# Optimization experiments

Measured on AMD Instinct MI355X. Metric: run time of the kernel, lower is better.

## Reference

```python
import jax, jax.numpy as jnp
import numpy as np

ED = 1024   # encoder_dim
GH = 1024   # gnn_hidden
NL = 3      # gnn_layers
NH = 8      # gnn_heads
HD = GH // NH
N = 2048    # graph nodes
B = 1024    # query/doc batch
TEMP = 0.05
LAPW = 0.1

def _layernorm(x, g, b):
    mu = jnp.mean(x, axis=-1, keepdims=True)
    var = jnp.mean((x - mu) ** 2, axis=-1, keepdims=True)
    return (x - mu) * jax.lax.rsqrt(var + 1e-5) * g + b

def _mlp_proj(x, W1, b1, g, beta, W2, b2):
    h = _layernorm(x @ W1 + b1, g, beta)
    h = jax.nn.gelu(h, approximate=False)
    return h @ W2 + b2

def _l2norm(x):
    n = jnp.linalg.norm(x, axis=-1, keepdims=True)
    return x / jnp.maximum(n, 1e-12)

def _gnn(x, adj, gatW, a1, a2, ln_g, ln_b, poW, pob):
    mask = adj > 0
    for l in range(NL):
        Wh = jnp.einsum('nf,hfo->hno', x, gatW[l])            # [H,N,HD]
        # a([Wh_i, Wh_j]) == Wh_i@a1 + Wh_j@a2 (linear, no bias): avoids NxNx2F concat
        s1 = jnp.einsum('hno,ho->hn', Wh, a1[l])
        s2 = jnp.einsum('hno,ho->hn', Wh, a2[l])
        e = jax.nn.leaky_relu(s1[:, :, None] + s2[:, None, :], 0.2)  # [H,N,N]
        att = jax.nn.softmax(jnp.where(mask[None], e, -9e15), axis=-1)
        h = jnp.einsum('hnm,hmo->hno', att, Wh)               # [H,N,HD]
        h = jnp.transpose(h, (1, 0, 2)).reshape(x.shape[0], GH)  # concat heads
        h = jax.nn.elu(_layernorm(h, ln_g[l], ln_b[l]))
        x = x + h  # in_features == hidden so residual applies every layer
    return x @ poW + pob

def _forward(query_embeds, pos_doc_embeds, node_embeds, adj, laplacian, params):
    (qW1, qb1, qg, qbt, qW2, qb2,
     dW1, db1, dg, dbt, dW2, db2,
     gatW, a1, a2, ln_g, ln_b, poW, pob) = params
    graph_embeds = _gnn(node_embeds, adj, gatW, a1, a2, ln_g, ln_b, poW, pob)
    q = _l2norm(_mlp_proj(query_embeds, qW1, qb1, qg, qbt, qW2, qb2))
    p = _l2norm(_mlp_proj(pos_doc_embeds, dW1, db1, dg, dbt, dW2, db2))
    pos_sim = jnp.sum(q * p, axis=-1) / TEMP                  # [B]
    neg_sim = (q @ p.T) / TEMP                                # [B,B]
    logits = jnp.concatenate([pos_sim[:, None], neg_sim], axis=1)
    info_nce = jnp.mean(jax.nn.logsumexp(logits, axis=-1) - logits[:, 0])
    lap = jnp.sum(graph_embeds * (laplacian @ graph_embeds)) / graph_embeds.shape[0]
    return info_nce + LAPW * lap, info_nce, lap

def setup_inputs() -> dict:
    key = jax.random.key(0)
    ks = jax.random.split(key, 24)
    r = lambda k, s: jax.random.normal(k, s, jnp.float32) * 0.02
    adj = (jax.random.uniform(ks[3], (N, N)) < 0.02).astype(jnp.float32)
    adj = jnp.maximum(adj, jnp.eye(N, dtype=jnp.float32))
    return {
        'query_embeds': jax.random.normal(ks[0], (B, ED), jnp.float32),
        'pos_doc_embeds': jax.random.normal(ks[1], (B, ED), jnp.float32),
        'node_embeds': jax.random.normal(ks[2], (N, ED), jnp.float32),
        'adj': adj,
        'laplacian': r(ks[4], (N, N)),
        'qW1': r(ks[5], (ED, ED)), 'qb1': jnp.zeros((ED,), jnp.float32),
        'qg': jnp.ones((ED,), jnp.float32), 'qbt': jnp.zeros((ED,), jnp.float32),
        'qW2': r(ks[6], (ED, ED)), 'qb2': jnp.zeros((ED,), jnp.float32),
        'dW1': r(ks[7], (ED, ED)), 'db1': jnp.zeros((ED,), jnp.float32),
        'dg': jnp.ones((ED,), jnp.float32), 'dbt': jnp.zeros((ED,), jnp.float32),
        'dW2': r(ks[8], (ED, ED)), 'db2': jnp.zeros((ED,), jnp.float32),
        'gatW': r(ks[9], (NL, NH, ED, HD)),
        'a1': r(ks[10], (NL, NH, HD)),
        'a2': r(ks[11], (NL, NH, HD)),
        'ln_g': jnp.ones((NL, GH), jnp.float32),
        'ln_b': jnp.zeros((NL, GH), jnp.float32),
        'poW': r(ks[12], (GH, ED)),
        'pob': jnp.zeros((ED,), jnp.float32),
    }

def reference(query_embeds, pos_doc_embeds, node_embeds, adj, laplacian,
              qW1, qb1, qg, qbt, qW2, qb2,
              dW1, db1, dg, dbt, dW2, db2,
              gatW, a1, a2, ln_g, ln_b, poW, pob):
    params = (qW1, qb1, qg, qbt, qW2, qb2,
              dW1, db1, dg, dbt, dW2, db2,
              gatW, a1, a2, ln_g, ln_b, poW, pob)
    return _forward(query_embeds, pos_doc_embeds, node_embeds, adj, laplacian, params)
```

## Files before the change

kernel.cpp:

```cpp
#include <hip/hip_runtime.h>
#include <math.h>

#define ED    1024
#define GH    1024
#define NLAY  3
#define NHEAD 8
#define HD    128
#define NNODE 2048
#define BQ    1024
#define CAP   192

typedef unsigned short u16;
typedef __attribute__((ext_vector_type(8))) short short8;
typedef __attribute__((ext_vector_type(4))) float f32x4;

static const size_t OFF_X    = 0;
static const size_t OFF_XB   = 2097152;
static const size_t OFF_WHB  = 3145728;
static const size_t OFF_WTG  = 4194304;
static const size_t OFF_WTPO = 5767168;
static const size_t OFF_WTQ1 = 6291456;
static const size_t OFF_WTD1 = 6815744;
static const size_t OFF_WTQ2 = 7340032;
static const size_t OFF_WTD2 = 7864320;
static const size_t OFF_G    = 8388608;
static const size_t OFF_GT   = 10485760;
static const size_t OFF_QPB  = 11534336;
static const size_t OFF_HF   = 12582912;
static const size_t OFF_HB   = 14680064;
static const size_t OFF_FF   = 15728640;
static const size_t OFF_FB   = 17825792;
static const size_t OFF_NEG  = 18874368;
static const size_t OFF_ACC  = 19922944;
static const size_t OFF_NCNT = 19922952;
static const size_t OFF_NBR  = 19925000;

__device__ __forceinline__ u16 f2bf(float f) {
  unsigned int u = __float_as_uint(f);
  return (u16)((u + 0x7fffu + ((u >> 16) & 1u)) >> 16);
}
__device__ __forceinline__ float bf2f(u16 u) {
  return __uint_as_float(((unsigned int)u) << 16);
}

__device__ __forceinline__ float waveSum(float v) {
#pragma unroll
  for (int off = 32; off; off >>= 1) v += __shfl_xor(v, off, 64);
  return v;
}
__device__ __forceinline__ float waveMax(float v) {
#pragma unroll
  for (int off = 32; off; off >>= 1) v = fmaxf(v, __shfl_xor(v, off, 64));
  return v;
}
__device__ __forceinline__ float blockSum(float v) {
  __shared__ float buf[4];
  int lane = threadIdx.x & 63, wid = threadIdx.x >> 6, nw = (blockDim.x + 63) >> 6;
  v = waveSum(v);
  __syncthreads();
  if (lane == 0) buf[wid] = v;
  __syncthreads();
  float r = buf[0];
  for (int i = 1; i < nw; ++i) r += buf[i];
  return r;
}
__device__ __forceinline__ float blockMax(float v) {
  __shared__ float buf[4];
  int lane = threadIdx.x & 63, wid = threadIdx.x >> 6, nw = (blockDim.x + 63) >> 6;
  v = waveMax(v);
  __syncthreads();
  if (lane == 0) buf[wid] = v;
  __syncthreads();
  float r = buf[0];
  for (int i = 1; i < nw; ++i) r = fmaxf(r, buf[i]);
  return r;
}

__global__ __launch_bounds__(256) void gemm128(
    const u16* __restrict__ A, const u16* __restrict__ B0,
    const u16* __restrict__ B1, float* __restrict__ C, u16* __restrict__ Cb,
    const float* __restrict__ bias0, const float* __restrict__ bias1,
    int M, int N, int K, int split, float scale) {
  __shared__ u16 As[2][128][32];
  __shared__ u16 Bs[2][128][32];
  const int tid = threadIdx.x, wave = tid >> 6, lane = tid & 63;
  const int bm = blockIdx.y * 128, bn = blockIdx.x * 128;
  const u16* Bt = (bm < split) ? B0 : B1;
  const float* bias = (bm < split) ? bias0 : bias1;

  const int sr = tid >> 2, ss = tid & 3;
  const u16* ga0 = A  + (size_t)(bm + sr) * K + ss * 8;
  const u16* ga1 = A  + (size_t)(bm + sr + 64) * K + ss * 8;
  const u16* gb0 = Bt + (size_t)(bn + sr) * K + ss * 8;
  const u16* gb1 = Bt + (size_t)(bn + sr + 64) * K + ss * 8;

  const int r16 = lane & 15, kg = lane >> 4;
  const int wm = (wave >> 1) * 64, wn = (wave & 1) * 64;

  f32x4 acc[4][4] = {};
  const int nk = K >> 5;

  float4 pa0 = *(const float4*)ga0;
  float4 pa1 = *(const float4*)ga1;
  float4 pb0 = *(const float4*)gb0;
  float4 pb1 = *(const float4*)gb1;

  for (int kt = 0; kt < nk; ++kt) {
    const int p = kt & 1;
    *(float4*)&As[p][sr][ss * 8]      = pa0;
    *(float4*)&As[p][sr + 64][ss * 8] = pa1;
    *(float4*)&Bs[p][sr][ss * 8]      = pb0;
    *(float4*)&Bs[p][sr + 64][ss * 8] = pb1;
    __syncthreads();
    if (kt + 1 < nk) {
      ga0 += 32; ga1 += 32; gb0 += 32; gb1 += 32;
      pa0 = *(const float4*)ga0;
      pa1 = *(const float4*)ga1;
      pb0 = *(const float4*)gb0;
      pb1 = *(const float4*)gb1;
    }
    short8 av[4], bv[4];
#pragma unroll
    for (int i = 0; i < 4; ++i)
      av[i] = *(const short8*)&As[p][wm + i * 16 + r16][kg * 8];
#pragma unroll
    for (int j = 0; j < 4; ++j)
      bv[j] = *(const short8*)&Bs[p][wn + j * 16 + r16][kg * 8];
#pragma unroll
    for (int i = 0; i < 4; ++i)
#pragma unroll
      for (int j = 0; j < 4; ++j)
        acc[i][j] = __builtin_amdgcn_mfma_f32_16x16x32_bf16(av[i], bv[j], acc[i][j], 0, 0, 0);
  }

  if (C) {
#pragma unroll
    for (int j = 0; j < 4; ++j) {
      int col = bn + wn + j * 16 + r16;
      float bvv = bias ? bias[col] : 0.f;
#pragma unroll
      for (int i = 0; i < 4; ++i) {
        int row0 = bm + wm + i * 16 + kg * 4;
        float* cp = C + (size_t)row0 * N + col;
#pragma unroll
        for (int r = 0; r < 4; ++r)
          cp[(size_t)r * N] = acc[i][j][r] * scale + bvv;
      }
    }
  }
  if (Cb) {
#pragma unroll
    for (int j = 0; j < 4; ++j) {
      int col = bn + wn + j * 16 + r16;
      float bvv = bias ? bias[col] : 0.f;
#pragma unroll
      for (int i = 0; i < 4; ++i) {
        int row0 = bm + wm + i * 16 + kg * 4;
        u16* cp = Cb + (size_t)row0 * N + col;
#pragma unroll
        for (int r = 0; r < 4; ++r)
          cp[(size_t)r * N] = f2bf(acc[i][j][r] * scale + bvv);
      }
    }
  }
}

__global__ __launch_bounds__(256) void gemm_dual(
    const u16* __restrict__ A0, const u16* __restrict__ B00,
    const u16* __restrict__ B01, float* __restrict__ C0, u16* __restrict__ D0,
    const float* __restrict__ e0, const float* __restrict__ f0, int M0, int sp0, float sc0,
    const u16* __restrict__ A1, const u16* __restrict__ B10,
    const u16* __restrict__ B11, float* __restrict__ C1, u16* __restrict__ D1,
    const float* __restrict__ e1, const float* __restrict__ f1, int M1, int sp1, float sc1) {
  const int z = blockIdx.z;
  const u16* A   = z ? A1 : A0;
  const u16* Bt0 = z ? B10 : B00;
  const u16* Bt1 = z ? B11 : B01;
  float* C = z ? C1 : C0;
  u16*   D = z ? D1 : D0;
  const float* bias0 = z ? e1 : e0;
  const float* bias1 = z ? f1 : f0;
  const int M = z ? M1 : M0, split = z ? sp1 : sp0;
  const float scale = z ? sc1 : sc0;
  const int bm = blockIdx.y * 128, bn = blockIdx.x * 128;
  if (bm >= M) return;
  const int N = 1024, K = 1024;
  const u16* Bt = (bm < split) ? Bt0 : Bt1;
  const float* bias = (bm < split) ? bias0 : bias1;

  __shared__ u16 As[2][128][32];
  __shared__ u16 Bs[2][128][32];
  const int tid = threadIdx.x, wave = tid >> 6, lane = tid & 63;
  const int sr = tid >> 2, ss = tid & 3;
  const u16* ga0 = A  + (size_t)(bm + sr) * K + ss * 8;
  const u16* ga1 = A  + (size_t)(bm + sr + 64) * K + ss * 8;
  const u16* gb0 = Bt + (size_t)(bn + sr) * K + ss * 8;
  const u16* gb1 = Bt + (size_t)(bn + sr + 64) * K + ss * 8;
  const int r16 = lane & 15, kg = lane >> 4;
  const int wm = (wave >> 1) * 64, wn = (wave & 1) * 64;

  f32x4 acc[4][4] = {};
  const int nk = 32;

  float4 pa0 = *(const float4*)ga0;
  float4 pa1 = *(const float4*)ga1;
  float4 pb0 = *(const float4*)gb0;
  float4 pb1 = *(const float4*)gb1;

  for (int kt = 0; kt < nk; ++kt) {
    const int p = kt & 1;
    *(float4*)&As[p][sr][ss * 8]      = pa0;
    *(float4*)&As[p][sr + 64][ss * 8] = pa1;
    *(float4*)&Bs[p][sr][ss * 8]      = pb0;
    *(float4*)&Bs[p][sr + 64][ss * 8] = pb1;
    __syncthreads();
    if (kt + 1 < nk) {
      ga0 += 32; ga1 += 32; gb0 += 32; gb1 += 32;
      pa0 = *(const float4*)ga0;
      pa1 = *(const float4*)ga1;
      pb0 = *(const float4*)gb0;
      pb1 = *(const float4*)gb1;
    }
    short8 av[4], bv[4];
#pragma unroll
    for (int i = 0; i < 4; ++i)
      av[i] = *(const short8*)&As[p][wm + i * 16 + r16][kg * 8];
#pragma unroll
    for (int j = 0; j < 4; ++j)
      bv[j] = *(const short8*)&Bs[p][wn + j * 16 + r16][kg * 8];
#pragma unroll
    for (int i = 0; i < 4; ++i)
#pragma unroll
      for (int j = 0; j < 4; ++j)
        acc[i][j] = __builtin_amdgcn_mfma_f32_16x16x32_bf16(av[i], bv[j], acc[i][j], 0, 0, 0);
  }

  if (C) {
#pragma unroll
    for (int j = 0; j < 4; ++j) {
      int col = bn + wn + j * 16 + r16;
      float bvv = bias ? bias[col] : 0.f;
#pragma unroll
      for (int i = 0; i < 4; ++i) {
        int row0 = bm + wm + i * 16 + kg * 4;
        float* cp = C + (size_t)row0 * N + col;
#pragma unroll
        for (int r = 0; r < 4; ++r)
          cp[(size_t)r * N] = acc[i][j][r] * scale + bvv;
      }
    }
  }
  if (D) {
#pragma unroll
    for (int j = 0; j < 4; ++j) {
      int col = bn + wn + j * 16 + r16;
      float bvv = bias ? bias[col] : 0.f;
#pragma unroll
      for (int i = 0; i < 4; ++i) {
        int row0 = bm + wm + i * 16 + kg * 4;
        u16* cp = D + (size_t)row0 * N + col;
#pragma unroll
        for (int r = 0; r < 4; ++r)
          cp[(size_t)r * N] = f2bf(acc[i][j][r] * scale + bvv);
      }
    }
  }
}

__global__ __launch_bounds__(256) void lap_gemm(
    const float* __restrict__ A, const u16* __restrict__ Bt,
    const float* __restrict__ G, float* __restrict__ acc_out) {
  __shared__ u16 As[2][128][32];
  __shared__ u16 Bs[2][128][32];
  const int tid = threadIdx.x, wave = tid >> 6, lane = tid & 63;
  const int n = blockIdx.x;
  const int member = n >> 6, gzy = n & 63;
  const int bm = (gzy & 15) * 128, bn = member * 128, k0 = (gzy >> 4) * 512;

  const int sr = tid >> 2, ss = tid & 3;
  const float* gA0 = A + (size_t)(bm + sr) * NNODE + k0 + ss * 8;
  const float* gA1 = gA0 + (size_t)64 * NNODE;
  const u16* gb0 = Bt + (size_t)(bn + sr) * NNODE + k0 + ss * 8;
  const u16* gb1 = Bt + (size_t)(bn + sr + 64) * NNODE + k0 + ss * 8;

  const int r16 = lane & 15, kg = lane >> 4;
  const int wm = (wave >> 1) * 64, wn = (wave & 1) * 64;

  f32x4 acc[4][4] = {};
  const int nk = 16;

  float4 a0l = *(const float4*)gA0, a0h = *(const float4*)(gA0 + 4);
  float4 a1l = *(const float4*)gA1, a1h = *(const float4*)(gA1 + 4);
  float4 pb0 = *(const float4*)gb0;
  float4 pb1 = *(const float4*)gb1;

  for (int kt = 0; kt < nk; ++kt) {
    const int p = kt & 1;
    {
      ushort4 lo, hi;
      lo.x = f2bf(a0l.x); lo.y = f2bf(a0l.y); lo.z = f2bf(a0l.z); lo.w = f2bf(a0l.w);
      hi.x = f2bf(a0h.x); hi.y = f2bf(a0h.y); hi.z = f2bf(a0h.z); hi.w = f2bf(a0h.w);
      *(ushort4*)&As[p][sr][ss * 8]     = lo;
      *(ushort4*)&As[p][sr][ss * 8 + 4] = hi;
      lo.x = f2bf(a1l.x); lo.y = f2bf(a1l.y); lo.z = f2bf(a1l.z); lo.w = f2bf(a1l.w);
      hi.x = f2bf(a1h.x); hi.y = f2bf(a1h.y); hi.z = f2bf(a1h.z); hi.w = f2bf(a1h.w);
      *(ushort4*)&As[p][sr + 64][ss * 8]     = lo;
      *(ushort4*)&As[p][sr + 64][ss * 8 + 4] = hi;
    }
    *(float4*)&Bs[p][sr][ss * 8]      = pb0;
    *(float4*)&Bs[p][sr + 64][ss * 8] = pb1;
    __syncthreads();
    if (kt + 1 < nk) {
      gA0 += 32; gA1 += 32; gb0 += 32; gb1 += 32;
      a0l = *(const float4*)gA0; a0h = *(const float4*)(gA0 + 4);
      a1l = *(const float4*)gA1; a1h = *(const float4*)(gA1 + 4);
      pb0 = *(const float4*)gb0;
      pb1 = *(const float4*)gb1;
    }
    short8 av[4], bv[4];
#pragma unroll
    for (int i = 0; i < 4; ++i)
      av[i] = *(const short8*)&As[p][wm + i * 16 + r16][kg * 8];
#pragma unroll
    for (int j = 0; j < 4; ++j)
      bv[j] = *(const short8*)&Bs[p][wn + j * 16 + r16][kg * 8];
#pragma unroll
    for (int i = 0; i < 4; ++i)
#pragma unroll
      for (int j = 0; j < 4; ++j)
        acc[i][j] = __builtin_amdgcn_mfma_f32_16x16x32_bf16(av[i], bv[j], acc[i][j], 0, 0, 0);
  }

  float sum = 0.f;
#pragma unroll
  for (int j = 0; j < 4; ++j) {
    int col = bn + wn + j * 16 + r16;
#pragma unroll
    for (int i = 0; i < 4; ++i) {
      int row0 = bm + wm + i * 16 + kg * 4;
      const float* gp = G + (size_t)row0 * ED + col;
#pragma unroll
      for (int r = 0; r < 4; ++r)
        sum += acc[i][j][r] * gp[(size_t)r * ED];
    }
  }
  sum = blockSum(sum);
  if (tid == 0) atomicAdd(acc_out, sum);
}

__global__ __launch_bounds__(256) void fused_att(
    const u16* __restrict__ WHb, const float* __restrict__ a1l,
    const float* __restrict__ a2l, const int* __restrict__ nbr,
    const int* __restrict__ ncnt, float* __restrict__ X, u16* __restrict__ Xb,
    const float* __restrict__ g, const float* __restrict__ b) {
  __shared__ int snb[CAP];
  const int n = blockIdx.x, t = threadIdx.x;
  const int cnt = ncnt[n];
  for (int j = t; j < cnt; j += 256) snb[j] = nbr[n * CAP + j];

  const float4 a1v = *(const float4*)(a1l + (t << 2));
  const float4 a2v = *(const float4*)(a2l + (t << 2));

  ushort4 w0 = *(const ushort4*)(WHb + ((size_t)n << 10) + (t << 2));
  float s1 = bf2f(w0.x) * a1v.x + bf2f(w0.y) * a1v.y +
             bf2f(w0.z) * a1v.z + bf2f(w0.w) * a1v.w;
#pragma unroll
  for (int off = 16; off; off >>= 1) s1 += __shfl_xor(s1, off, 64);

  __syncthreads();

  float mh = -1e30f, lh = 0.f;
  float ac0 = 0.f, ac1 = 0.f, ac2 = 0.f, ac3 = 0.f;
  ushort4 wx0 = *(const ushort4*)(WHb + ((size_t)snb[0] << 10) + (t << 2));
  ushort4 wx1 = wx0;
  if (cnt > 1) wx1 = *(const ushort4*)(WHb + ((size_t)snb[1] << 10) + (t << 2));
  int j = 0;
  for (; j + 1 < cnt; j += 2) {
    float va0 = bf2f(wx0.x), va1 = bf2f(wx0.y), va2 = bf2f(wx0.z), va3 = bf2f(wx0.w);
    float vb0 = bf2f(wx1.x), vb1 = bf2f(wx1.y), vb2 = bf2f(wx1.z), vb3 = bf2f(wx1.w);
    int j2 = (j + 2 < cnt) ? j + 2 : 0;
    int j3 = (j + 3 < cnt) ? j + 3 : 0;
    wx0 = *(const ushort4*)(WHb + ((size_t)snb[j2] << 10) + (t << 2));
    wx1 = *(const ushort4*)(WHb + ((size_t)snb[j3] << 10) + (t << 2));
    float s2a = va0 * a2v.x + va1 * a2v.y + va2 * a2v.z + va3 * a2v.w;
    float s2b = vb0 * a2v.x + vb1 * a2v.y + vb2 * a2v.z + vb3 * a2v.w;
#pragma unroll
    for (int off = 16; off; off >>= 1) {
      s2a += __shfl_xor(s2a, off, 64);
      s2b += __shfl_xor(s2b, off, 64);
    }
    float ea = s1 + s2a; ea = ea > 0.f ? ea : 0.2f * ea;
    float eb = s1 + s2b; eb = eb > 0.f ? eb : 0.2f * eb;
    float nm = fmaxf(mh, fmaxf(ea, eb));
    float al = __expf(mh - nm);
    float pa = __expf(ea - nm);
    float pb = __expf(eb - nm);
    lh = lh * al + pa + pb;
    ac0 = ac0 * al + pa * va0 + pb * vb0;
    ac1 = ac1 * al + pa * va1 + pb * vb1;
    ac2 = ac2 * al + pa * va2 + pb * vb2;
    ac3 = ac3 * al + pa * va3 + pb * vb3;
    mh = nm;
  }
  if (j < cnt) {
    float va0 = bf2f(wx0.x), va1 = bf2f(wx0.y), va2 = bf2f(wx0.z), va3 = bf2f(wx0.w);
    float s2 = va0 * a2v.x + va1 * a2v.y + va2 * a2v.z + va3 * a2v.w;
#pragma unroll
    for (int off = 16; off; off >>= 1) s2 += __shfl_xor(s2, off, 64);
    float e = s1 + s2; e = e > 0.f ? e : 0.2f * e;
    float nm = fmaxf(mh, e);
    float al = __expf(mh - nm), p = __expf(e - nm);
    lh = lh * al + p;
    ac0 = ac0 * al + p * va0;
    ac1 = ac1 * al + p * va1;
    ac2 = ac2 * al + p * va2;
    ac3 = ac3 * al + p * va3;
    mh = nm;
  }
  float inv = 1.f / lh;
  float o0 = ac0 * inv, o1 = ac1 * inv, o2 = ac2 * inv, o3 = ac3 * inv;

  float s  = o0 + o1 + o2 + o3;
  float sq = o0 * o0 + o1 * o1 + o2 * o2 + o3 * o3;
  float mean = blockSum(s) * (1.f / 1024.f);
  float var  = blockSum(sq) * (1.f / 1024.f) - mean * mean;
  float rstd = rsqrtf(fmaxf(var, 0.f) + 1e-5f);
  float4 xv = *(float4*)&X[((size_t)n << 10) + (t << 2)];
  float ov[4] = {o0, o1, o2, o3};
  float xa[4] = {xv.x, xv.y, xv.z, xv.w};
#pragma unroll
  for (int i = 0; i < 4; ++i) {
    int c = (t << 2) + i;
    float y = (ov[i] - mean) * rstd * g[c] + b[c];
    y = y > 0.f ? y : expm1f(y);
    xa[i] += y;
  }
  *(float4*)&X[((size_t)n << 10) + (t << 2)] = make_float4(xa[0], xa[1], xa[2], xa[3]);
  ushort4 o;
  o.x = f2bf(xa[0]); o.y = f2bf(xa[1]); o.z = f2bf(xa[2]); o.w = f2bf(xa[3]);
  *(ushort4*)&Xb[((size_t)n << 10) + (t << 2)] = o;
}

__global__ void build_nbr(const float* __restrict__ adj, int* __restrict__ nbr,
                          int* __restrict__ ncnt, float* __restrict__ acc) {
  __shared__ int cnt;
  int n = blockIdx.x, tid = threadIdx.x;
  if (n == 0 && tid < 2) acc[tid] = 0.f;
  if (tid == 0) cnt = 0;
  __syncthreads();
  for (int c = tid; c < NNODE; c += 256) {
    if (adj[((size_t)n << 11) + c] > 0.f) {
      int p = atomicAdd(&cnt, 1);
      if (p < CAP) nbr[n * CAP + p] = c;
    }
  }
  __syncthreads();
  if (tid == 0) ncnt[n] = cnt < CAP ? cnt : CAP;
}

__global__ __launch_bounds__(256) void cvt_dual(const float* __restrict__ in,
                                                float* __restrict__ Xf,
                                                u16* __restrict__ Xb) {
  int i = blockIdx.x * 256 + threadIdx.x;
  float4 v = ((const float4*)in)[i];
  ((float4*)Xf)[i] = v;
  ushort4 o;
  o.x = f2bf(v.x); o.y = f2bf(v.y); o.z = f2bf(v.z); o.w = f2bf(v.w);
  ((ushort4*)Xb)[i] = o;
}

__global__ __launch_bounds__(256) void qd_cvt(const float* __restrict__ q,
                                              const float* __restrict__ d,
                                              u16* __restrict__ out) {
  int i = blockIdx.x * 256 + threadIdx.x;
  const int half = BQ * ED / 4;
  const float* src = (i < half) ? q : d;
  int j = (i < half) ? i : i - half;
  float4 v = ((const float4*)src)[j];
  ushort4 o;
  o.x = f2bf(v.x); o.y = f2bf(v.y); o.z = f2bf(v.z); o.w = f2bf(v.w);
  ((ushort4*)out)[i] = o;
}

__global__ __launch_bounds__(256) void cvt_transpose(
    const float* __restrict__ in, u16* __restrict__ out,
    int R, int C, long inb, long outb) {
  __shared__ float T[64][65];
  const float* ip = in + (size_t)blockIdx.z * inb;
  u16* op = out + (size_t)blockIdx.z * outb;
  int r0 = blockIdx.y * 64, c0 = blockIdx.x * 64;
  int t = threadIdx.x;
#pragma unroll
  for (int p = 0; p < 4; ++p) {
    int row = p * 16 + (t >> 4), col = (t & 15) * 4;
    float4 v = *(const float4*)&ip[(size_t)(r0 + row) * C + c0 + col];
    T[row][col] = v.x; T[row][col + 1] = v.y;
    T[row][col + 2] = v.z; T[row][col + 3] = v.w;
  }
  __syncthreads();
#pragma unroll
  for (int p = 0; p < 4; ++p) {
    int c = p * 16 + (t >> 4), r = (t & 15) * 4;
    ushort4 o;
    o.x = f2bf(T[r][c]); o.y = f2bf(T[r + 1][c]);
    o.z = f2bf(T[r + 2][c]); o.w = f2bf(T[r + 3][c]);
    *(ushort4*)&op[(size_t)(c0 + c) * R + r0 + r] = o;
  }
}

__global__ __launch_bounds__(256) void ln_gelu(
    const float* __restrict__ IN, u16* __restrict__ OUT,
    const float* __restrict__ g0, const float* __restrict__ b0,
    const float* __restrict__ g1, const float* __restrict__ b1) {
  int row = blockIdx.x, tid = threadIdx.x;
  const float* g = (row < 1024) ? g0 : g1;
  const float* b = (row < 1024) ? b0 : b1;
  float4 v = *(const float4*)&IN[((size_t)row << 10) + (tid << 2)];
  float s = v.x + v.y + v.z + v.w;
  float sq = v.x * v.x + v.y * v.y + v.z * v.z + v.w * v.w;
  float mean = blockSum(s) * (1.f / 1024.f);
  float var = blockSum(sq) * (1.f / 1024.f) - mean * mean;
  float rstd = rsqrtf(fmaxf(var, 0.f) + 1e-5f);
  float vals[4] = {v.x, v.y, v.z, v.w};
  ushort4 o;
  u16* oa = (u16*)&o;
#pragma unroll
  for (int i = 0; i < 4; ++i) {
    int c = (tid << 2) + i;
    float y = (vals[i] - mean) * rstd * g[c] + b[c];
    y = 0.5f * y * (1.f + erff(y * 0.70710678118654752f));
    oa[i] = f2bf(y);
  }
  *(ushort4*)&OUT[((size_t)row << 10) + (tid << 2)] = o;
}

__global__ __launch_bounds__(256) void l2norm_k(const float* __restrict__ IN,
                                                u16* __restrict__ OUT) {
  int row = blockIdx.x, tid = threadIdx.x;
  float4 v = *(const float4*)&IN[((size_t)row << 10) + (tid << 2)];
  float sq = v.x * v.x + v.y * v.y + v.z * v.z + v.w * v.w;
  float s = blockSum(sq);
  float inv = 1.f / fmaxf(sqrtf(s), 1e-12f);
  ushort4 o;
  o.x = f2bf(v.x * inv); o.y = f2bf(v.y * inv);
  o.z = f2bf(v.z * inv); o.w = f2bf(v.w * inv);
  *(ushort4*)&OUT[((size_t)row << 10) + (tid << 2)] = o;
}

__global__ __launch_bounds__(256) void lse_kernel(const float* __restrict__ NEG,
                                                  float* __restrict__ acc) {
  int bq = blockIdx.x, tid = threadIdx.x;
  const float* row = NEG + ((size_t)bq << 10);
  float4 v = *(const float4*)&row[tid << 2];
  float lm = fmaxf(fmaxf(v.x, v.y), fmaxf(v.z, v.w));
  float m = blockMax(lm);
  float ls = __expf(v.x - m) + __expf(v.y - m) + __expf(v.z - m) + __expf(v.w - m);
  float ssum = blockSum(ls);
  if (tid == 0) {
    float pos = row[bq];
    float loss = m + logf(ssum + __expf(pos - m)) - pos;
    atomicAdd(acc + 1, loss);
  }
}

__global__ void final_kernel(const float* __restrict__ acc, float* __restrict__ out) {
  float lap = acc[0] / 2048.f;
  float info = acc[1] / 1024.f;
  out[0] = info + 0.1f * lap;
  out[1] = info;
  out[2] = lap;
}

extern "C" void kernel_launch(void* const* d_in, const int* in_sizes, int n_in,
                              void* d_out, int out_size, void* d_ws, size_t ws_size,
                              hipStream_t stream) {
  const float* query = (const float*)d_in[0];
  const float* docs  = (const float*)d_in[1];
  const float* nodes = (const float*)d_in[2];
  const float* adj   = (const float*)d_in[3];
  const float* lapl  = (const float*)d_in[4];
  const float* qW1 = (const float*)d_in[5],  *qb1 = (const float*)d_in[6];
  const float* qg  = (const float*)d_in[7],  *qbt = (const float*)d_in[8];
  const float* qW2 = (const float*)d_in[9],  *qb2 = (const float*)d_in[10];
  const float* dW1 = (const float*)d_in[11], *db1 = (const float*)d_in[12];
  const float* dg  = (const float*)d_in[13], *dbt = (const float*)d_in[14];
  const float* dW2 = (const float*)d_in[15], *db2 = (const float*)d_in[16];
  const float* gatW = (const float*)d_in[17];
  const float* a1   = (const float*)d_in[18];
  const float* a2   = (const float*)d_in[19];
  const float* ln_g = (const float*)d_in[20];
  const float* ln_b = (const float*)d_in[21];
  const float* poW  = (const float*)d_in[22];
  const float* pob  = (const float*)d_in[23];
  float* out = (float*)d_out;

  float* ws = (float*)d_ws;
  float* X    = ws + OFF_X;
  u16*   Xb   = (u16*)(ws + OFF_XB);
  u16*   WHb  = (u16*)(ws + OFF_WHB);
  u16*   WtG  = (u16*)(ws + OFF_WTG);
  u16*   WtPO = (u16*)(ws + OFF_WTPO);
  u16*   WtQ1 = (u16*)(ws + OFF_WTQ1);
  u16*   WtD1 = (u16*)(ws + OFF_WTD1);
  u16*   WtQ2 = (u16*)(ws + OFF_WTQ2);
  u16*   WtD2 = (u16*)(ws + OFF_WTD2);
  float* G    = ws + OFF_G;
  u16*   Gt   = (u16*)(ws + OFF_GT);
  u16*   QPb  = (u16*)(ws + OFF_QPB);
  float* Hf   = ws + OFF_HF;
  u16*   Hb   = (u16*)(ws + OFF_HB);
  float* Ff   = ws + OFF_FF;
  u16*   Fb   = (u16*)(ws + OFF_FB);
  float* NEG  = ws + OFF_NEG;
  float* ACC  = ws + OFF_ACC;
  int*   NCNT = (int*)(ws + OFF_NCNT);
  int*   NBR  = (int*)(ws + OFF_NBR);

  const size_t WSL = (size_t)GH * ED;

  build_nbr<<<NNODE, 256, 0, stream>>>(adj, NBR, NCNT, ACC);
  cvt_dual<<<2048, 256, 0, stream>>>(nodes, X, Xb);
  qd_cvt<<<2048, 256, 0, stream>>>(query, docs, QPb);
  cvt_transpose<<<dim3(2, 16, 24), 256, 0, stream>>>(
      gatW, WtG, ED, HD, (long)ED * HD, (long)HD * ED);
  cvt_transpose<<<dim3(16, 16, 1), 256, 0, stream>>>(poW, WtPO, GH, ED, 0, 0);
  cvt_transpose<<<dim3(16, 16, 1), 256, 0, stream>>>(qW1, WtQ1, ED, ED, 0, 0);
  cvt_transpose<<<dim3(16, 16, 1), 256, 0, stream>>>(dW1, WtD1, ED, ED, 0, 0);
  cvt_transpose<<<dim3(16, 16, 1), 256, 0, stream>>>(qW2, WtQ2, ED, ED, 0, 0);
  cvt_transpose<<<dim3(16, 16, 1), 256, 0, stream>>>(dW2, WtD2, ED, ED, 0, 0);

  gemm_dual<<<dim3(8, 16, 2), 256, 0, stream>>>(
      Xb, WtG, WtG, nullptr, WHb, nullptr, nullptr, NNODE, NNODE, 1.f,
      QPb, WtQ1, WtD1, Hf, nullptr, qb1, db1, 2 * BQ, BQ, 1.f);
  fused_att<<<NNODE, 256, 0, stream>>>(WHb, a1, a2, NBR, NCNT, X, Xb, ln_g, ln_b);
  ln_gelu<<<2 * BQ, 256, 0, stream>>>(Hf, Hb, qg, qbt, dg, dbt);

  gemm_dual<<<dim3(8, 16, 2), 256, 0, stream>>>(
      Xb, WtG + WSL, WtG + WSL, nullptr, WHb, nullptr, nullptr, NNODE, NNODE, 1.f,
      Hb, WtQ2, WtD2, Ff, nullptr, qb2, db2, 2 * BQ, BQ, 1.f);
  fused_att<<<NNODE, 256, 0, stream>>>(WHb, a1 + NHEAD * HD, a2 + NHEAD * HD,
      NBR, NCNT, X, Xb, ln_g + GH, ln_b + GH);
  l2norm_k<<<2 * BQ, 256, 0, stream>>>(Ff, Fb);

  gemm_dual<<<dim3(8, 16, 2), 256, 0, stream>>>(
      Xb, WtG + 2 * WSL, WtG + 2 * WSL, nullptr, WHb, nullptr, nullptr, NNODE, NNODE, 1.f,
      Fb, Fb + (size_t)BQ * ED, Fb + (size_t)BQ * ED, NEG, nullptr,
      nullptr, nullptr, BQ, BQ, 20.f);
  fused_att<<<NNODE, 256, 0, stream>>>(WHb, a1 + 2 * NHEAD * HD, a2 + 2 * NHEAD * HD,
      NBR, NCNT, X, Xb, ln_g + 2 * GH, ln_b + 2 * GH);
  lse_kernel<<<BQ, 256, 0, stream>>>(NEG, ACC);

  gemm128<<<dim3(ED / 128, NNODE / 128), 256, 0, stream>>>(
      Xb, WtPO, WtPO, G, nullptr, pob, pob, NNODE, ED, GH, NNODE, 1.f);
  cvt_transpose<<<dim3(16, 32, 1), 256, 0, stream>>>(G, Gt, NNODE, ED, 0, 0);
  lap_gemm<<<512, 256, 0, stream>>>(lapl, Gt, G, ACC);

  final_kernel<<<1, 1, 0, stream>>>(ACC, out);
}
```

Measured before the change: 418.4 us.

## Fuse GAT score projections into GEMM epilogue and restructure attention aggregation

The per-head attention scores s1/s2 are now computed in the Wh GEMM epilogue from the fp32 accumulators via warp shuffles and shared-memory reduction, and written to small buffers. The attention kernel then reads precomputed scores, does a two-pass softmax per head, and aggregates neighbours in batches of 8 loads instead of an online-softmax loop with per-neighbour dot-product reductions. Separately, the five weight transposes are merged into one launch, and the projection GEMM writes a transposed bf16 copy directly, removing a transpose kernel. Scores now come from fp32 accumulators rather than bf16-rounded Wh, which slightly changes numerics. The ev[6] array also assumes at most 192 neighbours.

```diff
diff --git a/kernel.cpp b/kernel.cpp
--- a/kernel.cpp
+++ b/kernel.cpp
@@ -31,9 +31,11 @@
 static const size_t OFF_FF   = 15728640;
 static const size_t OFF_FB   = 17825792;
 static const size_t OFF_NEG  = 18874368;
-static const size_t OFF_ACC  = 19922944;
-static const size_t OFF_NCNT = 19922952;
-static const size_t OFF_NBR  = 19925000;
+static const size_t OFF_SV1  = 19922944;
+static const size_t OFF_SV2  = 19939328;
+static const size_t OFF_ACC  = 19955712;
+static const size_t OFF_NCNT = 19955720;
+static const size_t OFF_NBR  = 19957768;
 
 __device__ __forceinline__ u16 f2bf(float f) {
   unsigned int u = __float_as_uint(f);
@@ -79,6 +81,7 @@
 __global__ __launch_bounds__(256) void gemm128(
     const u16* __restrict__ A, const u16* __restrict__ B0,
     const u16* __restrict__ B1, float* __restrict__ C, u16* __restrict__ Cb,
+    u16* __restrict__ Ct,
     const float* __restrict__ bias0, const float* __restrict__ bias1,
     int M, int N, int K, int split, float scale) {
   __shared__ u16 As[2][128][32];
@@ -163,12 +166,31 @@
       }
     }
   }
+  if (Ct) {
+#pragma unroll
+    for (int j = 0; j < 4; ++j) {
+      int col = bn + wn + j * 16 + r16;
+      float bvv = bias ? bias[col] : 0.f;
+#pragma unroll
+      for (int i = 0; i < 4; ++i) {
+        int row0 = bm + wm + i * 16 + kg * 4;
+        ushort4 o;
+        o.x = f2bf(acc[i][j][0] * scale + bvv);
+        o.y = f2bf(acc[i][j][1] * scale + bvv);
+        o.z = f2bf(acc[i][j][2] * scale + bvv);
+        o.w = f2bf(acc[i][j][3] * scale + bvv);
+        *(ushort4*)&Ct[(size_t)col * M + row0] = o;
+      }
+    }
+  }
 }
 
 __global__ __launch_bounds__(256) void gemm_dual(
     const u16* __restrict__ A0, const u16* __restrict__ B00,
     const u16* __restrict__ B01, float* __restrict__ C0, u16* __restrict__ D0,
     const float* __restrict__ e0, const float* __restrict__ f0, int M0, int sp0, float sc0,
+    const float* __restrict__ A1v, const float* __restrict__ A2v,
+    float* __restrict__ S1o, float* __restrict__ S2o,
     const u16* __restrict__ A1, const u16* __restrict__ B10,
     const u16* __restrict__ B11, float* __restrict__ C1, u16* __restrict__ D1,
     const float* __restrict__ e1, const float* __restrict__ f1, int M1, int sp1, float sc1) {
@@ -265,6 +287,53 @@
       }
     }
   }
+
+  if (z == 0 && S1o) {
+    float c1[4], c2[4];
+#pragma unroll
+    for (int j = 0; j < 4; ++j) {
+      int col = bn + wn + j * 16 + r16;
+      c1[j] = A1v[col]; c2[j] = A2v[col];
+    }
+    float r1[4][4], r2[4][4];
+#pragma unroll
+    for (int i = 0; i < 4; ++i)
+#pragma unroll
+      for (int r = 0; r < 4; ++r) {
+        float v1 = 0.f, v2 = 0.f;
+#pragma unroll
+        for (int j = 0; j < 4; ++j) {
+          v1 += acc[i][j][r] * c1[j];
+          v2 += acc[i][j][r] * c2[j];
+        }
+#pragma unroll
+        for (int off = 8; off; off >>= 1) {
+          v1 += __shfl_xor(v1, off, 64);
+          v2 += __shfl_xor(v2, off, 64);
+        }
+        r1[i][r] = v1; r2[i][r] = v2;
+      }
+    __syncthreads();
+    float* sb1 = (float*)&As[0][0][0];
+    float* sb2 = sb1 + 256;
+    if (r16 == 0) {
+      int half = wn >> 6;
+#pragma unroll
+      for (int i = 0; i < 4; ++i)
+#pragma unroll
+        for (int r = 0; r < 4; ++r) {
+          int row = wm + i * 16 + kg * 4 + r;
+          sb1[half * 128 + row] = r1[i][r];
+          sb2[half * 128 + row] = r2[i][r];
+        }
+    }
+    __syncthreads();
+    if (tid < 128) {
+      int h = blockIdx.x;
+      S1o[(h << 11) + bm + tid] = sb1[tid] + sb1[128 + tid];
+      S2o[(h << 11) + bm + tid] = sb2[tid] + sb2[128 + tid];
+    }
+  }
 }
 
 __global__ __launch_bounds__(256) void lap_gemm(
@@ -349,76 +418,62 @@
 }
 
 __global__ __launch_bounds__(256) void fused_att(
-    const u16* __restrict__ WHb, const float* __restrict__ a1l,
-    const float* __restrict__ a2l, const int* __restrict__ nbr,
+    const u16* __restrict__ WHb, const float* __restrict__ S1,
+    const float* __restrict__ S2, const int* __restrict__ nbr,
     const int* __restrict__ ncnt, float* __restrict__ X, u16* __restrict__ Xb,
     const float* __restrict__ g, const float* __restrict__ b) {
   __shared__ int snb[CAP];
+  __shared__ float pw[NHEAD][CAP];
   const int n = blockIdx.x, t = threadIdx.x;
+  const int h = t >> 5, l = t & 31;
   const int cnt = ncnt[n];
+  const int cntP = (cnt + 7) & ~7;
   for (int j = t; j < cnt; j += 256) snb[j] = nbr[n * CAP + j];
-
-  const float4 a1v = *(const float4*)(a1l + (t << 2));
-  const float4 a2v = *(const float4*)(a2l + (t << 2));
-
-  ushort4 w0 = *(const ushort4*)(WHb + ((size_t)n << 10) + (t << 2));
-  float s1 = bf2f(w0.x) * a1v.x + bf2f(w0.y) * a1v.y +
-             bf2f(w0.z) * a1v.z + bf2f(w0.w) * a1v.w;
-#pragma unroll
-  for (int off = 16; off; off >>= 1) s1 += __shfl_xor(s1, off, 64);
-
-  __syncthreads();
-
-  float mh = -1e30f, lh = 0.f;
-  float ac0 = 0.f, ac1 = 0.f, ac2 = 0.f, ac3 = 0.f;
-  ushort4 wx0 = *(const ushort4*)(WHb + ((size_t)snb[0] << 10) + (t << 2));
-  ushort4 wx1 = wx0;
-  if (cnt > 1) wx1 = *(const ushort4*)(WHb + ((size_t)snb[1] << 10) + (t << 2));
-  int j = 0;
-  for (; j + 1 < cnt; j += 2) {
-    float va0 = bf2f(wx0.x), va1 = bf2f(wx0.y), va2 = bf2f(wx0.z), va3 = bf2f(wx0.w);
-    float vb0 = bf2f(wx1.x), vb1 = bf2f(wx1.y), vb2 = bf2f(wx1.z), vb3 = bf2f(wx1.w);
-    int j2 = (j + 2 < cnt) ? j + 2 : 0;
-    int j3 = (j + 3 < cnt) ? j + 3 : 0;
-    wx0 = *(const ushort4*)(WHb + ((size_t)snb[j2] << 10) + (t << 2));
-    wx1 = *(const ushort4*)(WHb + ((size_t)snb[j3] << 10) + (t << 2));
-    float s2a = va0 * a2v.x + va1 * a2v.y + va2 * a2v.z + va3 * a2v.w;
-    float s2b = vb0 * a2v.x + vb1 * a2v.y + vb2 * a2v.z + vb3 * a2v.w;
-#pragma unroll
-    for (int off = 16; off; off >>= 1) {
-      s2a += __shfl_xor(s2a, off, 64);
-      s2b += __shfl_xor(s2b, off, 64);
-    }
-    float ea = s1 + s2a; ea = ea > 0.f ? ea : 0.2f * ea;
-    float eb = s1 + s2b; eb = eb > 0.f ? eb : 0.2f * eb;
-    float nm = fmaxf(mh, fmaxf(ea, eb));
-    float al = __expf(mh - nm);
-    float pa = __expf(ea - nm);
-    float pb = __expf(eb - nm);
-    lh = lh * al + pa + pb;
-    ac0 = ac0 * al + pa * va0 + pb * vb0;
-    ac1 = ac1 * al + pa * va1 + pb * vb1;
-    ac2 = ac2 * al + pa * va2 + pb * vb2;
-    ac3 = ac3 * al + pa * va3 + pb * vb3;
-    mh = nm;
-  }
-  if (j < cnt) {
-    float va0 = bf2f(wx0.x), va1 = bf2f(wx0.y), va2 = bf2f(wx0.z), va3 = bf2f(wx0.w);
-    float s2 = va0 * a2v.x + va1 * a2v.y + va2 * a2v.z + va3 * a2v.w;
-#pragma unroll
-    for (int off = 16; off; off >>= 1) s2 += __shfl_xor(s2, off, 64);
-    float e = s1 + s2; e = e > 0.f ? e : 0.2f * e;
-    float nm = fmaxf(mh, e);
-    float al = __expf(mh - nm), p = __expf(e - nm);
-    lh = lh * al + p;
-    ac0 = ac0 * al + p * va0;
-    ac1 = ac1 * al + p * va1;
-    ac2 = ac2 * al + p * va2;
-    ac3 = ac3 * al + p * va3;
-    mh = nm;
-  }
-  float inv = 1.f / lh;
-  float o0 = ac0 * inv, o1 = ac1 * inv, o2 = ac2 * inv, o3 = ac3 * inv;
+  __syncthreads();
+  for (int j = cnt + t; j < cntP; j += 256) snb[j] = snb[0];
+
+  const float s1v = S1[(h << 11) + n];
+  float ev[6];
+  float lmax = -1e30f;
+  int ne = 0;
+  for (int j = l; j < cnt; j += 32) {
+    float e = s1v + S2[(h << 11) + snb[j]];
+    e = e > 0.f ? e : 0.2f * e;
+    ev[ne++] = e;
+    lmax = fmaxf(lmax, e);
+  }
+#pragma unroll
+  for (int off = 16; off; off >>= 1) lmax = fmaxf(lmax, __shfl_xor(lmax, off, 64));
+  float lsum = 0.f;
+  ne = 0;
+  for (int j = l; j < cnt; j += 32) {
+    float p = __expf(ev[ne++] - lmax);
+    pw[h][j] = p;
+    lsum += p;
+  }
+  for (int j = cnt + l; j < cntP; j += 32) pw[h][j] = 0.f;
+#pragma unroll
+  for (int off = 16; off; off >>= 1) lsum += __shfl_xor(lsum, off, 64);
+  const float inv = 1.f / lsum;
+  __syncthreads();
+
+  float o0 = 0.f, o1 = 0.f, o2 = 0.f, o3 = 0.f;
+  const u16* wp = WHb + (t << 2);
+  for (int j0 = 0; j0 < cntP; j0 += 8) {
+    ushort4 buf[8];
+#pragma unroll
+    for (int u = 0; u < 8; ++u)
+      buf[u] = *(const ushort4*)(wp + ((size_t)snb[j0 + u] << 10));
+#pragma unroll
+    for (int u = 0; u < 8; ++u) {
+      float w = pw[h][j0 + u];
+      o0 += w * bf2f(buf[u].x);
+      o1 += w * bf2f(buf[u].y);
+      o2 += w * bf2f(buf[u].z);
+      o3 += w * bf2f(buf[u].w);
+    }
+  }
+  o0 *= inv; o1 *= inv; o2 *= inv; o3 *= inv;
 
   float s  = o0 + o1 + o2 + o3;
   float sq = o0 * o0 + o1 * o1 + o2 * o2 + o3 * o3;
@@ -482,12 +537,8 @@
   ((ushort4*)out)[i] = o;
 }
 
-__global__ __launch_bounds__(256) void cvt_transpose(
-    const float* __restrict__ in, u16* __restrict__ out,
-    int R, int C, long inb, long outb) {
+__device__ __forceinline__ void cvt_tr_body(const float* ip, u16* op, int R, int C) {
   __shared__ float T[64][65];
-  const float* ip = in + (size_t)blockIdx.z * inb;
-  u16* op = out + (size_t)blockIdx.z * outb;
   int r0 = blockIdx.y * 64, c0 = blockIdx.x * 64;
   int t = threadIdx.x;
 #pragma unroll
@@ -506,6 +557,29 @@
     o.z = f2bf(T[r + 2][c]); o.w = f2bf(T[r + 3][c]);
     *(ushort4*)&op[(size_t)(c0 + c) * R + r0 + r] = o;
   }
+}
+
+__global__ __launch_bounds__(256) void cvt_transpose(
+    const float* __restrict__ in, u16* __restrict__ out,
+    int R, int C, long inb, long outb) {
+  cvt_tr_body(in + (size_t)blockIdx.z * inb, out + (size_t)blockIdx.z * outb, R, C);
+}
+
+__global__ __launch_bounds__(256) void cvt_transpose5(
+    const float* __restrict__ i0, u16* __restrict__ o0,
+    const float* __restrict__ i1, u16* __restrict__ o1,
+    const float* __restrict__ i2, u16* __restrict__ o2,
+    const float* __restrict__ i3, u16* __restrict__ o3,
+    const float* __restrict__ i4, u16* __restrict__ o4) {
+  const float* in; u16* out;
+  switch (blockIdx.z) {
+    case 0: in = i0; out = o0; break;
+    case 1: in = i1; out = o1; break;
+    case 2: in = i2; out = o2; break;
+    case 3: in = i3; out = o3; break;
+    default: in = i4; out = o4; break;
+  }
+  cvt_tr_body(in, out, 1024, 1024);
 }
 
 __global__ __launch_bounds__(256) void ln_gelu(
@@ -612,6 +686,8 @@
   float* Ff   = ws + OFF_FF;
   u16*   Fb   = (u16*)(ws + OFF_FB);
   float* NEG  = ws + OFF_NEG;
+  float* S1v  = ws + OFF_SV1;
+  float* S2v  = ws + OFF_SV2;
   float* ACC  = ws + OFF_ACC;
   int*   NCNT = (int*)(ws + OFF_NCNT);
   int*   NBR  = (int*)(ws + OFF_NBR);
@@ -623,36 +699,35 @@
   qd_cvt<<<2048, 256, 0, stream>>>(query, docs, QPb);
   cvt_transpose<<<dim3(2, 16, 24), 256, 0, stream>>>(
       gatW, WtG, ED, HD, (long)ED * HD, (long)HD * ED);
-  cvt_transpose<<<dim3(16, 16, 1), 256, 0, stream>>>(poW, WtPO, GH, ED, 0, 0);
-  cvt_transpose<<<dim3(16, 16, 1), 256, 0, stream>>>(qW1, WtQ1, ED, ED, 0, 0);
-  cvt_transpose<<<dim3(16, 16, 1), 256, 0, stream>>>(dW1, WtD1, ED, ED, 0, 0);
-  cvt_transpose<<<dim3(16, 16, 1), 256, 0, stream>>>(qW2, WtQ2, ED, ED, 0, 0);
-  cvt_transpose<<<dim3(16, 16, 1), 256, 0, stream>>>(dW2, WtD2, ED, ED, 0, 0);
+  cvt_transpose5<<<dim3(16, 16, 5), 256, 0, stream>>>(
+      poW, WtPO, qW1, WtQ1, dW1, WtD1, qW2, WtQ2, dW2, WtD2);
 
   gemm_dual<<<dim3(8, 16, 2), 256, 0, stream>>>(
       Xb, WtG, WtG, nullptr, WHb, nullptr, nullptr, NNODE, NNODE, 1.f,
+      a1, a2, S1v, S2v,
       QPb, WtQ1, WtD1, Hf, nullptr, qb1, db1, 2 * BQ, BQ, 1.f);
-  fused_att<<<NNODE, 256, 0, stream>>>(WHb, a1, a2, NBR, NCNT, X, Xb, ln_g, ln_b);
+  fused_att<<<NNODE, 256, 0, stream>>>(WHb, S1v, S2v, NBR, NCNT, X, Xb, ln_g, ln_b);
   ln_gelu<<<2 * BQ, 256, 0, stream>>>(Hf, Hb, qg, qbt, dg, dbt);
 
   gemm_dual<<<dim3(8, 16, 2), 256, 0, stream>>>(
       Xb, WtG + WSL, WtG + WSL, nullptr, WHb, nullptr, nullptr, NNODE, NNODE, 1.f,
+      a1 + NHEAD * HD, a2 + NHEAD * HD, S1v, S2v,
       Hb, WtQ2, WtD2, Ff, nullptr, qb2, db2, 2 * BQ, BQ, 1.f);
-  fused_att<<<NNODE, 256, 0, stream>>>(WHb, a1 + NHEAD * HD, a2 + NHEAD * HD,
-      NBR, NCNT, X, Xb, ln_g + GH, ln_b + GH);
+  fused_att<<<NNODE, 256, 0, stream>>>(WHb, S1v, S2v, NBR, NCNT, X, Xb,
+      ln_g + GH, ln_b + GH);
   l2norm_k<<<2 * BQ, 256, 0, stream>>>(Ff, Fb);
 
   gemm_dual<<<dim3(8, 16, 2), 256, 0, stream>>>(
       Xb, WtG + 2 * WSL, WtG + 2 * WSL, nullptr, WHb, nullptr, nullptr, NNODE, NNODE, 1.f,
+      a1 + 2 * NHEAD * HD, a2 + 2 * NHEAD * HD, S1v, S2v,
       Fb, Fb + (size_t)BQ * ED, Fb + (size_t)BQ * ED, NEG, nullptr,
       nullptr, nullptr, BQ, BQ, 20.f);
-  fused_att<<<NNODE, 256, 0, stream>>>(WHb, a1 + 2 * NHEAD * HD, a2 + 2 * NHEAD * HD,
-      NBR, NCNT, X, Xb, ln_g + 2 * GH, ln_b + 2 * GH);
+  fused_att<<<NNODE, 256, 0, stream>>>(WHb, S1v, S2v, NBR, NCNT, X, Xb,
+      ln_g + 2 * GH, ln_b + 2 * GH);
   lse_kernel<<<BQ, 256, 0, stream>>>(NEG, ACC);
 
   gemm128<<<dim3(ED / 128, NNODE / 128), 256, 0, stream>>>(
-      Xb, WtPO, WtPO, G, nullptr, pob, pob, NNODE, ED, GH, NNODE, 1.f);
-  cvt_transpose<<<dim3(16, 32, 1), 256, 0, stream>>>(G, Gt, NNODE, ED, 0, 0);
+      Xb, WtPO, WtPO, G, nullptr, Gt, pob, pob, NNODE, ED, GH, NNODE, 1.f);
   lap_gemm<<<512, 256, 0, stream>>>(lapl, Gt, G, ACC);
 
   final_kernel<<<1, 1, 0, stream>>>(ACC, out);
```

After: 381.8 us. -8.8%, faster.
